# Performance work log

Measured on AMD Instinct MI355X. Metric: run time of the kernel, lower is better.

The kernel has to match this reference:

```python
import jax, jax.numpy as jnp
import numpy as np

N, C_IN, C_OUT, H = 4096, 1024, 512, 4
D = C_OUT // H  # per-head output dim
TEMP = 1.0


def setup_inputs() -> dict:
    key = jax.random.key(0)
    ks = jax.random.split(key, 6)
    node_feats = jax.random.normal(ks[0], (N, C_IN), dtype=jnp.float32)
    # sparse 0/1 adjacency mask, avg degree ~ 0.02*N
    adj_matrix = jax.random.bernoulli(ks[1], 0.02, (N, N)).astype(jnp.float32)
    lim_w = np.sqrt(6.0 / (C_IN + D))
    lim_v = np.sqrt(6.0 / (D + 1))
    W = jax.random.uniform(ks[2], (H, C_IN, D), jnp.float32, -lim_w, lim_w)
    b = jnp.zeros((H, D), dtype=jnp.float32)
    v0 = jax.random.uniform(ks[3], (H, D), jnp.float32, -lim_v, lim_v)
    v1 = jax.random.uniform(ks[4], (H, D), jnp.float32, -lim_v, lim_v)
    return {"node_feats": node_feats, "adj_matrix": adj_matrix,
            "W": W, "b": b, "v0": v0, "v1": v1}


def reference(node_feats, adj_matrix, W, b, v0, v1):
    # per-head linear projection: [H, N, D]
    h = jnp.einsum('nc,hcd->hnd', node_feats, W) + b[:, None, :]
    f1 = jnp.einsum('hnd,hd->hn', h, v0)  # [H, N]
    f2 = jnp.einsum('hnd,hd->hn', h, v1)  # [H, N]
    logits = adj_matrix[None, :, :] * (f1[:, :, None] + f2[:, None, :])
    # torch to_sparse drops exact zeros; sparse.softmax normalizes over
    # the remaining (nonzero) entries only, zeros stay zero when densified.
    mask = logits != 0
    vals = (jax.nn.sigmoid(logits) - 0.5) / TEMP
    rowmax = jnp.max(jnp.where(mask, vals, -1e30), axis=-1, keepdims=True)
    e = jnp.where(mask, jnp.exp(vals - rowmax), 0.0)
    denom = jnp.sum(e, axis=-1, keepdims=True)
    p = jnp.where(denom > 0, e / jnp.maximum(denom, 1e-30), 0.0)
    out = jnp.einsum('hnm,hmd->hnd', p, h)  # [H, N, D]
    # concat heads along feature dim -> [N, H*D]
    return out.transpose(1, 0, 2).reshape(node_feats.shape[0], -1)
```

## Files before the change

kernel.cpp:

```cpp
#include <hip/hip_runtime.h>
#include <hip/hip_bf16.h>

#define N_NODES 4096
#define C_IN    1024
#define H_HEADS 4
#define D_HEAD  128
#define C_OUT   512
#define DEG_CAP 256

typedef __attribute__((ext_vector_type(8))) short short8;
typedef __attribute__((ext_vector_type(8))) unsigned short u16x8;
typedef __attribute__((ext_vector_type(4))) float f32x4;

__device__ __forceinline__ unsigned short f2bf(float f) {
    unsigned u = __float_as_uint(f);
    u += 0x7FFFu + ((u >> 16) & 1u);
    return (unsigned short)(u >> 16);
}
__device__ __forceinline__ float bf2f(unsigned short u) {
    return __uint_as_float((unsigned)u << 16);
}
__device__ __forceinline__ float sigv(float s) {
    return 1.f / (1.f + __expf(-s)) - 0.5f;
}

#define GLOAD_LDS16(gp, lp)                                                        \
    __builtin_amdgcn_global_load_lds(                                              \
        (const __attribute__((address_space(1))) unsigned int*)(gp),               \
        (__attribute__((address_space(3))) unsigned int*)(lp), 16, 0, 0)

__global__ void k_cvt(const float* __restrict__ X, const float* __restrict__ W,
                      unsigned short* __restrict__ Xb, unsigned short* __restrict__ Wt) {
    if (blockIdx.x < 2048) {
        int g = blockIdx.x * blockDim.x + threadIdx.x;
        const float4* s = (const float4*)(X + (size_t)g * 8);
        float4 a = s[0], b = s[1];
        ushort4 p0, p1;
        p0.x = f2bf(a.x); p0.y = f2bf(a.y); p0.z = f2bf(a.z); p0.w = f2bf(a.w);
        p1.x = f2bf(b.x); p1.y = f2bf(b.y); p1.z = f2bf(b.z); p1.w = f2bf(b.w);
        ushort4* d = (ushort4*)(Xb + (size_t)g * 8);
        d[0] = p0; d[1] = p1;
    } else {
        int g = (blockIdx.x - 2048) * blockDim.x + threadIdx.x;
        int o = g * 4;
        int c  = o & 1023;
        int hd = o >> 10;
        int d  = hd & 127;
        int h  = hd >> 7;
        const float* src = W + (size_t)h * C_IN * D_HEAD + (size_t)c * D_HEAD + d;
        ushort4 p;
        p.x = f2bf(src[0 * D_HEAD]);
        p.y = f2bf(src[1 * D_HEAD]);
        p.z = f2bf(src[2 * D_HEAD]);
        p.w = f2bf(src[3 * D_HEAD]);
        *(ushort4*)(Wt + o) = p;
    }
}

__global__ void k_gemm(const unsigned short* __restrict__ Xb,
                       const unsigned short* __restrict__ Wt,
                       const float* __restrict__ bias, unsigned short* __restrict__ Hb) {
    __shared__ __align__(16) unsigned short ldsA[2 * 64 * 64];
    __shared__ __align__(16) unsigned short ldsB[2 * 64 * 64];
    const int t    = threadIdx.x;
    const int lane = t & 63;
    const int wid  = t >> 6;
    const int wrow = wid >> 1, wcol = wid & 1;
    const int bid  = blockIdx.x;
    const int lin  = (bid & 7) * 64 + (bid >> 3);
    const int rowStart = (lin >> 3) * 64;
    const int colStart = (lin & 7) * 64;

    f32x4 acc[2][2];
#pragma unroll
    for (int m = 0; m < 2; ++m)
#pragma unroll
        for (int n = 0; n < 2; ++n) acc[m][n] = (f32x4){0.f, 0.f, 0.f, 0.f};

    const int lrow = lane >> 2;
    const int lkq  = lane & 3;

    auto stage = [&](int buf, int k0) {
#pragma unroll
        for (int ii = 0; ii < 2; ++ii) {
            int c  = wid * 2 + ii;
            int h  = c >> 2, rb = c & 3;
            const unsigned short* g =
                Xb + (size_t)(rowStart + rb * 16 + lrow) * C_IN + k0 + h * 32 + lkq * 8;
            GLOAD_LDS16(g, ldsA + buf * 4096 + h * 2048 + rb * 512);
        }
#pragma unroll
        for (int ii = 0; ii < 2; ++ii) {
            int c  = wid * 2 + ii;
            int h  = c >> 2, db = c & 3;
            const unsigned short* g =
                Wt + (size_t)(colStart + db * 16 + lrow) * C_IN + k0 + h * 32 + lkq * 8;
            GLOAD_LDS16(g, ldsB + buf * 4096 + h * 2048 + db * 512);
        }
    };

    stage(0, 0);
    __syncthreads();

    const int fo = (lane >> 4) * 8;
    const int fr = lane & 15;
    int cur = 0;
    for (int kt = 0; kt < 16; ++kt) {
        if (kt < 15) stage(cur ^ 1, (kt + 1) * 64);
        const unsigned short* __restrict__ lA = ldsA + cur * 4096;
        const unsigned short* __restrict__ lB = ldsB + cur * 4096;
#pragma unroll
        for (int h = 0; h < 2; ++h) {
            short8 bfr[2];
#pragma unroll
            for (int n = 0; n < 2; ++n)
                bfr[n] = *(const short8*)(lB + h * 2048 + (wcol * 32 + n * 16 + fr) * 32 + fo);
#pragma unroll
            for (int m = 0; m < 2; ++m) {
                short8 a = *(const short8*)(lA + h * 2048 + (wrow * 32 + m * 16 + fr) * 32 + fo);
#pragma unroll
                for (int n = 0; n < 2; ++n)
                    acc[m][n] = __builtin_amdgcn_mfma_f32_16x16x32_bf16(a, bfr[n], acc[m][n], 0, 0, 0);
            }
        }
        __syncthreads();
        cur ^= 1;
    }

#pragma unroll
    for (int m = 0; m < 2; ++m) {
        int row_g = rowStart + wrow * 32 + m * 16 + (lane >> 4) * 4;
#pragma unroll
        for (int n = 0; n < 2; ++n) {
            int col_g = colStart + wcol * 32 + n * 16 + (lane & 15);
            float bb = bias[col_g];
#pragma unroll
            for (int r = 0; r < 4; ++r)
                Hb[(size_t)(row_g + r) * C_OUT + col_g] = f2bf(acc[m][n][r] + bb);
        }
    }
}

__global__ void k_f12(const unsigned short* __restrict__ Hb, const float* __restrict__ v0,
                      const float* __restrict__ v1, float* __restrict__ F1,
                      float* __restrict__ F2) {
    const int t    = threadIdx.x;
    const int lane = t & 63;
    const int wid  = t >> 6;
    const int row  = blockIdx.x * 4 + wid;
    const int c0   = lane * 8;

    u16x8 hv = *(const u16x8*)(Hb + (size_t)row * C_OUT + c0);
    float4 va0 = *(const float4*)(v0 + c0), va1 = *(const float4*)(v0 + c0 + 4);
    float4 vb0 = *(const float4*)(v1 + c0), vb1 = *(const float4*)(v1 + c0 + 4);
    float h[8];
#pragma unroll
    for (int k = 0; k < 8; ++k) h[k] = bf2f(hv[k]);
    float s1 = h[0]*va0.x + h[1]*va0.y + h[2]*va0.z + h[3]*va0.w
             + h[4]*va1.x + h[5]*va1.y + h[6]*va1.z + h[7]*va1.w;
    float s2 = h[0]*vb0.x + h[1]*vb0.y + h[2]*vb0.z + h[3]*vb0.w
             + h[4]*vb1.x + h[5]*vb1.y + h[6]*vb1.z + h[7]*vb1.w;
#pragma unroll
    for (int off = 8; off; off >>= 1) {
        s1 += __shfl_xor(s1, off);
        s2 += __shfl_xor(s2, off);
    }
    if ((lane & 15) == 0) {
        int head = lane >> 4;
        F1[row * 4 + head] = s1;
        F2[row * 4 + head] = s2;
    }
}

__global__ void k_attn2(const float* __restrict__ adj, const unsigned short* __restrict__ Hb,
                        const float* __restrict__ F1, const float* __restrict__ F2,
                        float* __restrict__ Out) {
    __shared__ unsigned short jl[DEG_CAP];
    __shared__ float ev[DEG_CAP * 4];
    __shared__ float partial[4][C_OUT];
    __shared__ float dred[4][4];
    __shared__ int   wtot[4];

    const int i    = blockIdx.x;
    const int t    = threadIdx.x;
    const int lane = t & 63;
    const int wid  = t >> 6;
    const int headl = lane >> 4;

    const float4* arow = (const float4*)(adj + (size_t)i * N_NODES);
    float4 av[4];
#pragma unroll
    for (int r = 0; r < 4; ++r) av[r] = arow[r * 256 + t];
    float4 f1v = *(const float4*)(F1 + i * 4);

    int cnt = 0;
#pragma unroll
    for (int r = 0; r < 4; ++r)
        cnt += (av[r].x != 0.f) + (av[r].y != 0.f) + (av[r].z != 0.f) + (av[r].w != 0.f);
    int v = cnt;
#pragma unroll
    for (int off = 1; off < 64; off <<= 1) {
        int u = __shfl_up(v, off);
        if (lane >= off) v += u;
    }
    if (lane == 63) wtot[wid] = v;
    __syncthreads();
    int wpre = 0, total = 0;
#pragma unroll
    for (int w = 0; w < 4; ++w) {
        int tw = wtot[w];
        if (w < wid) wpre += tw;
        total += tw;
    }
    const int nv = min(total, DEG_CAP);
    int off = wpre + v - cnt;
#pragma unroll
    for (int r = 0; r < 4; ++r) {
        int j0 = (r * 256 + t) * 4;
        if (av[r].x != 0.f) { if (off < DEG_CAP) jl[off] = (unsigned short)j0;       off++; }
        if (av[r].y != 0.f) { if (off < DEG_CAP) jl[off] = (unsigned short)(j0 + 1); off++; }
        if (av[r].z != 0.f) { if (off < DEG_CAP) jl[off] = (unsigned short)(j0 + 2); off++; }
        if (av[r].w != 0.f) { if (off < DEG_CAP) jl[off] = (unsigned short)(j0 + 3); off++; }
    }
    __syncthreads();

    float e0 = 0.f, e1 = 0.f, e2 = 0.f, e3 = 0.f;
    if (t < nv) {
        int j = jl[t];
        float4 f2v = *(const float4*)(F2 + j * 4);
        float s0 = f1v.x + f2v.x, s1 = f1v.y + f2v.y;
        float s2 = f1v.z + f2v.z, s3 = f1v.w + f2v.w;
        e0 = (s0 != 0.f) ? __expf(sigv(s0)) : 0.f;
        e1 = (s1 != 0.f) ? __expf(sigv(s1)) : 0.f;
        e2 = (s2 != 0.f) ? __expf(sigv(s2)) : 0.f;
        e3 = (s3 != 0.f) ? __expf(sigv(s3)) : 0.f;
        ev[t * 4 + 0] = e0; ev[t * 4 + 1] = e1;
        ev[t * 4 + 2] = e2; ev[t * 4 + 3] = e3;
    }
#pragma unroll
    for (int o2 = 32; o2; o2 >>= 1) {
        e0 += __shfl_xor(e0, o2); e1 += __shfl_xor(e1, o2);
        e2 += __shfl_xor(e2, o2); e3 += __shfl_xor(e3, o2);
    }
    if (lane == 0) {
        dred[wid][0] = e0; dred[wid][1] = e1; dred[wid][2] = e2; dred[wid][3] = e3;
    }
    __syncthreads();

    float acc0[8], acc1[8];
#pragma unroll
    for (int k = 0; k < 8; ++k) { acc0[k] = 0.f; acc1[k] = 0.f; }
    const unsigned short* __restrict__ hp = Hb + lane * 8;

    int jj = wid;
#pragma unroll 4
    for (; jj + 4 < nv; jj += 8) {
        int ja = jl[jj], jb = jl[jj + 4];
        float ea = ev[jj * 4 + headl];
        float eb = ev[(jj + 4) * 4 + headl];
        u16x8 ha = *(const u16x8*)(hp + (size_t)ja * C_OUT);
        u16x8 hb = *(const u16x8*)(hp + (size_t)jb * C_OUT);
#pragma unroll
        for (int k = 0; k < 8; ++k) acc0[k] += ea * bf2f(ha[k]);
#pragma unroll
        for (int k = 0; k < 8; ++k) acc1[k] += eb * bf2f(hb[k]);
    }
    if (jj < nv) {
        int ja = jl[jj];
        float ea = ev[jj * 4 + headl];
        u16x8 ha = *(const u16x8*)(hp + (size_t)ja * C_OUT);
#pragma unroll
        for (int k = 0; k < 8; ++k) acc0[k] += ea * bf2f(ha[k]);
    }

    f32x4 lo = {acc0[0] + acc1[0], acc0[1] + acc1[1], acc0[2] + acc1[2], acc0[3] + acc1[3]};
    f32x4 hi = {acc0[4] + acc1[4], acc0[5] + acc1[5], acc0[6] + acc1[6], acc0[7] + acc1[7]};
    *(f32x4*)&partial[wid][lane * 8]     = lo;
    *(f32x4*)&partial[wid][lane * 8 + 4] = hi;
    __syncthreads();

    int head = t >> 6;
    float dn = dred[0][head] + dred[1][head] + dred[2][head] + dred[3][head];
    int c = 2 * t;
    float s0 = partial[0][c] + partial[1][c] + partial[2][c] + partial[3][c];
    float s1 = partial[0][c + 1] + partial[1][c + 1] + partial[2][c + 1] + partial[3][c + 1];
    float2 o;
    if (dn > 0.f) {
        float inv = 1.f / fmaxf(dn, 1e-30f);
        o.x = s0 * inv;
        o.y = s1 * inv;
    } else {
        o.x = 0.f; o.y = 0.f;
    }
    *(float2*)(Out + (size_t)i * C_OUT + c) = o;
}

extern "C" void kernel_launch(void* const* d_in, const int* in_sizes, int n_in,
                              void* d_out, int out_size, void* d_ws, size_t ws_size,
                              hipStream_t stream) {
    const float* X   = (const float*)d_in[0];
    const float* adj = (const float*)d_in[1];
    const float* W   = (const float*)d_in[2];
    const float* b   = (const float*)d_in[3];
    const float* v0  = (const float*)d_in[4];
    const float* v1  = (const float*)d_in[5];
    float* out = (float*)d_out;

    char* ws = (char*)d_ws;
    unsigned short* Wt  = (unsigned short*)ws;
    unsigned short* Xb  = (unsigned short*)(ws + (size_t)1 * 1024 * 1024);
    unsigned short* Hb  = (unsigned short*)(ws + (size_t)9 * 1024 * 1024);
    float*          F1  = (float*)(ws + (size_t)13 * 1024 * 1024);
    float*          F2  = F1 + N_NODES * 4;

    k_cvt<<<2560, 256, 0, stream>>>(X, W, Xb, Wt);
    k_gemm<<<512, 256, 0, stream>>>(Xb, Wt, b, Hb);
    k_f12<<<N_NODES / 4, 256, 0, stream>>>(Hb, v0, v1, F1, F2);
    k_attn2<<<N_NODES, 256, 0, stream>>>(adj, Hb, F1, F2, out);
}
```

Baseline: 61.68 us.

## Fuse f1/f2 projection into GEMM epilogue and swizzle LDS reads

Result: slower. 71.03 us (+15.2%).

```diff
diff --git a/kernel.cpp b/kernel.cpp
--- a/kernel.cpp
+++ b/kernel.cpp
@@ -59,7 +59,10 @@
 
 __global__ void k_gemm(const unsigned short* __restrict__ Xb,
                        const unsigned short* __restrict__ Wt,
-                       const float* __restrict__ bias, unsigned short* __restrict__ Hb) {
+                       const float* __restrict__ bias,
+                       const float* __restrict__ v0, const float* __restrict__ v1,
+                       unsigned short* __restrict__ Hb,
+                       float* __restrict__ F1, float* __restrict__ F2) {
     __shared__ __align__(16) unsigned short ldsA[2 * 64 * 64];
     __shared__ __align__(16) unsigned short ldsB[2 * 64 * 64];
     const int t    = threadIdx.x;
@@ -78,7 +81,7 @@
         for (int n = 0; n < 2; ++n) acc[m][n] = (f32x4){0.f, 0.f, 0.f, 0.f};
 
     const int lrow = lane >> 2;
-    const int lkq  = lane & 3;
+    const int lkq  = (lane & 3) ^ ((lane >> 3) & 3);
 
     auto stage = [&](int buf, int k0) {
 #pragma unroll
@@ -102,8 +105,8 @@
     stage(0, 0);
     __syncthreads();
 
-    const int fo = (lane >> 4) * 8;
     const int fr = lane & 15;
+    const int sw = ((lane >> 4) ^ ((fr >> 1) & 3)) * 8;
     int cur = 0;
     for (int kt = 0; kt < 16; ++kt) {
         if (kt < 15) stage(cur ^ 1, (kt + 1) * 64);
@@ -114,10 +117,10 @@
             short8 bfr[2];
 #pragma unroll
             for (int n = 0; n < 2; ++n)
-                bfr[n] = *(const short8*)(lB + h * 2048 + (wcol * 32 + n * 16 + fr) * 32 + fo);
+                bfr[n] = *(const short8*)(lB + h * 2048 + (wcol * 32 + n * 16 + fr) * 32 + sw);
 #pragma unroll
             for (int m = 0; m < 2; ++m) {
-                short8 a = *(const short8*)(lA + h * 2048 + (wrow * 32 + m * 16 + fr) * 32 + fo);
+                short8 a = *(const short8*)(lA + h * 2048 + (wrow * 32 + m * 16 + fr) * 32 + sw);
 #pragma unroll
                 for (int n = 0; n < 2; ++n)
                     acc[m][n] = __builtin_amdgcn_mfma_f32_16x16x32_bf16(a, bfr[n], acc[m][n], 0, 0, 0);
@@ -127,48 +130,33 @@
         cur ^= 1;
     }
 
+    const int c0 = colStart + wcol * 32 + (lane & 15);
+    const int c1 = c0 + 16;
+    const int head = c0 >> 7;
+    const float bb0 = bias[c0], bb1 = bias[c1];
+    const float v0c0 = v0[c0], v0c1 = v0[c1];
+    const float v1c0 = v1[c0], v1c1 = v1[c1];
 #pragma unroll
     for (int m = 0; m < 2; ++m) {
         int row_g = rowStart + wrow * 32 + m * 16 + (lane >> 4) * 4;
 #pragma unroll
-        for (int n = 0; n < 2; ++n) {
-            int col_g = colStart + wcol * 32 + n * 16 + (lane & 15);
-            float bb = bias[col_g];
-#pragma unroll
-            for (int r = 0; r < 4; ++r)
-                Hb[(size_t)(row_g + r) * C_OUT + col_g] = f2bf(acc[m][n][r] + bb);
+        for (int r = 0; r < 4; ++r) {
+            float h0 = acc[m][0][r] + bb0;
+            float h1 = acc[m][1][r] + bb1;
+            Hb[(size_t)(row_g + r) * C_OUT + c0] = f2bf(h0);
+            Hb[(size_t)(row_g + r) * C_OUT + c1] = f2bf(h1);
+            float p1 = h0 * v0c0 + h1 * v0c1;
+            float p2 = h0 * v1c0 + h1 * v1c1;
+#pragma unroll
+            for (int off = 8; off; off >>= 1) {
+                p1 += __shfl_xor(p1, off);
+                p2 += __shfl_xor(p2, off);
+            }
+            if ((lane & 15) == 0) {
+                atomicAdd(&F1[(row_g + r) * 4 + head], p1);
+                atomicAdd(&F2[(row_g + r) * 4 + head], p2);
+            }
         }
-    }
-}
-
-__global__ void k_f12(const unsigned short* __restrict__ Hb, const float* __restrict__ v0,
-                      const float* __restrict__ v1, float* __restrict__ F1,
-                      float* __restrict__ F2) {
-    const int t    = threadIdx.x;
-    const int lane = t & 63;
-    const int wid  = t >> 6;
-    const int row  = blockIdx.x * 4 + wid;
-    const int c0   = lane * 8;
-
-    u16x8 hv = *(const u16x8*)(Hb + (size_t)row * C_OUT + c0);
-    float4 va0 = *(const float4*)(v0 + c0), va1 = *(const float4*)(v0 + c0 + 4);
-    float4 vb0 = *(const float4*)(v1 + c0), vb1 = *(const float4*)(v1 + c0 + 4);
-    float h[8];
-#pragma unroll
-    for (int k = 0; k < 8; ++k) h[k] = bf2f(hv[k]);
-    float s1 = h[0]*va0.x + h[1]*va0.y + h[2]*va0.z + h[3]*va0.w
-             + h[4]*va1.x + h[5]*va1.y + h[6]*va1.z + h[7]*va1.w;
-    float s2 = h[0]*vb0.x + h[1]*vb0.y + h[2]*vb0.z + h[3]*vb0.w
-             + h[4]*vb1.x + h[5]*vb1.y + h[6]*vb1.z + h[7]*vb1.w;
-#pragma unroll
-    for (int off = 8; off; off >>= 1) {
-        s1 += __shfl_xor(s1, off);
-        s2 += __shfl_xor(s2, off);
-    }
-    if ((lane & 15) == 0) {
-        int head = lane >> 4;
-        F1[row * 4 + head] = s1;
-        F2[row * 4 + head] = s2;
     }
 }
 
@@ -313,8 +301,8 @@
     float*          F1  = (float*)(ws + (size_t)13 * 1024 * 1024);
     float*          F2  = F1 + N_NODES * 4;
 
+    hipMemsetAsync(F1, 0, 2 * N_NODES * 4 * sizeof(float), stream);
     k_cvt<<<2560, 256, 0, stream>>>(X, W, Xb, Wt);
-    k_gemm<<<512, 256, 0, stream>>>(Xb, Wt, b, Hb);
-    k_f12<<<N_NODES / 4, 256, 0, stream>>>(Hb, v0, v1, F1, F2);
+    k_gemm<<<512, 256, 0, stream>>>(Xb, Wt, b, v0, v1, Hb, F1, F2);
     k_attn2<<<N_NODES, 256, 0, stream>>>(adj, Hb, F1, F2, out);
 }
```
